# Performance work log

Hardware: AMD Instinct MI355X
Metric: run time of the kernel (lower is better)

## Reference

```python
import jax, jax.numpy as jnp
import numpy as np

B, S, D, H = 2, 2048, 1024, 16
DK = D // H


def setup_inputs() -> dict:
    key = jax.random.key(0)
    ks = jax.random.split(key, 12)
    s = 1.0 / np.sqrt(D)
    return {
        "query": jax.random.normal(ks[0], (B, S, D), dtype=jnp.float32),
        "key": jax.random.normal(ks[1], (B, S, D), dtype=jnp.float32),
        "value": jax.random.normal(ks[2], (B, S, D), dtype=jnp.float32),
        "mask": jax.random.randint(ks[3], (B, 1, 1, S), 0, 2, dtype=jnp.int32),
        "wq": jax.random.normal(ks[4], (D, D), dtype=jnp.float32) * s,
        "bq": jnp.zeros((D,), dtype=jnp.float32),
        "wk": jax.random.normal(ks[5], (D, D), dtype=jnp.float32) * s,
        "bk": jnp.zeros((D,), dtype=jnp.float32),
        "wv": jax.random.normal(ks[6], (D, D), dtype=jnp.float32) * s,
        "bv": jnp.zeros((D,), dtype=jnp.float32),
        "wo": jax.random.normal(ks[7], (D, D), dtype=jnp.float32) * s,
        "bo": jnp.zeros((D,), dtype=jnp.float32),
    }


def reference(query, key, value, mask, wq, bq, wk, bk, wv, bv, wo, bo):
    b, s, d = query.shape
    # torch Linear: y = x @ W^T + b, then split heads -> [B, H, S, dk]
    def proj(x, w, bias):
        return (x @ w.T + bias).reshape(b, -1, H, DK).transpose(0, 2, 1, 3)

    q = proj(query, wq, bq)
    k = proj(key, wk, bk)
    v = proj(value, wv, bv)

    scores = jnp.einsum("bhqd,bhkd->bhqk", q, k) / jnp.sqrt(jnp.float32(DK))
    scores = jnp.where(mask == 0, jnp.float32(-1e9), scores)
    attn = jax.nn.softmax(scores, axis=-1)  # [B,H,S,S]
    x = jnp.einsum("bhqk,bhkd->bhqd", attn, v)
    x = x.transpose(0, 2, 1, 3).reshape(b, s, d)
    return x @ wo.T + bo
```

## Files before the change

### kernel.cpp

```cpp
#include <hip/hip_runtime.h>
#include <math.h>

#define B_  2
#define S_  2048
#define D_  1024
#define H_  16
#define DK_ 64
#define NT_ (S_ / 64)

typedef unsigned short u16;
typedef unsigned int u32;
typedef __bf16 bf16x8 __attribute__((ext_vector_type(8)));
typedef float f32x4 __attribute__((ext_vector_type(4)));

typedef const __attribute__((address_space(1))) void* gas1_t;
typedef __attribute__((address_space(3))) void* las3_t;

__device__ __forceinline__ void gload_lds16(const void* g, void* l) {
    __builtin_amdgcn_global_load_lds((gas1_t)g, (las3_t)l, 16, 0, 0);
}

__device__ __forceinline__ u16 f2bf(float f) {
    union { float f; unsigned u; } v; v.f = f;
    return (u16)((v.u + 0x7fffu + ((v.u >> 16) & 1u)) >> 16);
}

__device__ __forceinline__ u32 pack_bf16_2(float lo, float hi) {
    union { float f; u32 u; } a, b;
    a.f = lo; b.f = hi;
    return __builtin_amdgcn_perm(b.u + 0x8000u, a.u + 0x8000u, 0x07060302u);
}

__global__ __launch_bounds__(256)
void cast_all(const float* __restrict__ q, const float* __restrict__ k,
              const float* __restrict__ v, const float* __restrict__ wq,
              const float* __restrict__ wk, const float* __restrict__ wv,
              const float* __restrict__ wo,
              u16* __restrict__ qb, u16* __restrict__ kb, u16* __restrict__ vb,
              u16* __restrict__ wqb, u16* __restrict__ wkb, u16* __restrict__ wvb,
              u16* __restrict__ wob)
{
    const int i = blockIdx.x * 256 + threadIdx.x;
    const float* src; u16* dst; int off;
    if (i < 3 * 1048576) {
        const int seg = i >> 20; off = i & 1048575;
        src = (seg == 0) ? q : (seg == 1) ? k : v;
        dst = (seg == 0) ? qb : (seg == 1) ? kb : vb;
    } else {
        const int j = i - 3 * 1048576;
        const int seg = j >> 18; off = j & 262143;
        src = (seg == 0) ? wq : (seg == 1) ? wk : (seg == 2) ? wv : wo;
        dst = (seg == 0) ? wqb : (seg == 1) ? wkb : (seg == 2) ? wvb : wob;
    }
    const float4 val = ((const float4*)src)[off];
    uint2 o;
    o.x = pack_bf16_2(val.x, val.y);
    o.y = pack_bf16_2(val.z, val.w);
    ((uint2*)dst)[off] = o;
}

template<int BN>
__device__ __forceinline__ void gemm_body(
    const u16* __restrict__ A, const u16* __restrict__ W,
    const float* __restrict__ bias, void* __restrict__ outp,
    float scale, int mode)
{
    constexpr int NJ = BN / 32;
    __shared__ u16 sA[128 * 32];
    __shared__ u16 sW[BN * 32];

    const int tid  = threadIdx.x;
    const int wave = tid >> 6, lane = tid & 63;
    const int quad = lane >> 4, l16 = lane & 15;
    const int m0 = blockIdx.y * 128;
    const int n0 = blockIdx.x * BN;
    const int wm = (wave >> 1) * 64;
    const int wn = (wave & 1) * (BN / 2);
    const int lrow = lane >> 2;
    const int lcol = (lane & 3) * 8;

    f32x4 acc[4][NJ];
    const f32x4 zero = {0.f, 0.f, 0.f, 0.f};
#pragma unroll
    for (int i = 0; i < 4; ++i)
#pragma unroll
        for (int j = 0; j < NJ; ++j) acc[i][j] = zero;

    for (int k0 = 0; k0 < D_; k0 += 32) {
        const int t0 = wave, t1 = wave + 4;
        gload_lds16(A + (size_t)(m0 + t0 * 16 + lrow) * D_ + k0 + lcol, sA + t0 * 512);
        gload_lds16(A + (size_t)(m0 + t1 * 16 + lrow) * D_ + k0 + lcol, sA + t1 * 512);
        if (BN == 128) {
            gload_lds16(W + (size_t)(n0 + t0 * 16 + lrow) * D_ + k0 + lcol, sW + t0 * 512);
            gload_lds16(W + (size_t)(n0 + t1 * 16 + lrow) * D_ + k0 + lcol, sW + t1 * 512);
        } else {
            gload_lds16(W + (size_t)(n0 + wave * 16 + lrow) * D_ + k0 + lcol, sW + wave * 512);
        }
        __syncthreads();

        bf16x8 af[4], bfr[NJ];
#pragma unroll
        for (int i = 0; i < 4; ++i)
            af[i] = *(const bf16x8*)(sA + (wm + i * 16 + l16) * 32 + quad * 8);
#pragma unroll
        for (int j = 0; j < NJ; ++j)
            bfr[j] = *(const bf16x8*)(sW + (wn + j * 16 + l16) * 32 + quad * 8);
#pragma unroll
        for (int i = 0; i < 4; ++i)
#pragma unroll
            for (int j = 0; j < NJ; ++j)
                acc[i][j] = __builtin_amdgcn_mfma_f32_16x16x32_bf16(af[i], bfr[j], acc[i][j], 0, 0, 0);
        __syncthreads();
    }

#pragma unroll
    for (int i = 0; i < 4; ++i) {
#pragma unroll
        for (int j = 0; j < NJ; ++j) {
            const int n = n0 + wn + j * 16 + l16;
            const float bn = bias[n];
            if (mode == 2) {
                const int mbase = m0 + wm + i * 16 + quad * 4;
                const int b = mbase >> 11, s = mbase & (S_ - 1);
                const int h = n >> 6, dk = n & 63;
                uint2 o;
                o.x = pack_bf16_2(acc[i][j][0] + bn, acc[i][j][1] + bn);
                o.y = pack_bf16_2(acc[i][j][2] + bn, acc[i][j][3] + bn);
                *(uint2*)((u16*)outp + (((size_t)(b * H_ + h)) * DK_ + dk) * S_ + s) = o;
            } else {
#pragma unroll
                for (int r = 0; r < 4; ++r) {
                    const int m = m0 + wm + i * 16 + quad * 4 + r;
                    const float v = acc[i][j][r] + bn;
                    if (mode == 0) {
                        ((float*)outp)[(size_t)m * D_ + n] = v;
                    } else {
                        const u16 hv = f2bf(v * scale);
                        const int b = m >> 11, s = m & (S_ - 1);
                        const int h = n >> 6, dk = n & 63;
                        ((u16*)outp)[(((size_t)(b * H_ + h)) * S_ + s) * DK_ + dk] = hv;
                    }
                }
            }
        }
    }
}

__global__ __launch_bounds__(256)
void qkv_gemm(const u16* __restrict__ qin, const u16* __restrict__ kin, const u16* __restrict__ vin,
              const u16* __restrict__ wqb, const u16* __restrict__ wkb, const u16* __restrict__ wvb,
              const float* __restrict__ bq, const float* __restrict__ bk, const float* __restrict__ bv,
              u16* __restrict__ Qp, u16* __restrict__ Kp, u16* __restrict__ Vp)
{
    const int z = blockIdx.z;
    const u16* A = (z == 0) ? qin : (z == 1) ? kin : vin;
    const u16* W = (z == 0) ? wqb : (z == 1) ? wkb : wvb;
    const float* bias = (z == 0) ? bq : (z == 1) ? bk : bv;
    u16* outp = (z == 0) ? Qp : (z == 1) ? Kp : Vp;
    const float scale = (z == 0) ? 0.18033688011112042f : 1.0f;
    const int mode = (z == 2) ? 2 : 1;
    gemm_body<128>(A, W, bias, outp, scale, mode);
}

__global__ __launch_bounds__(256)
void out_gemm(const u16* __restrict__ Xc, const u16* __restrict__ wob,
              const float* __restrict__ bo, float* __restrict__ out)
{
    gemm_body<128>(Xc, wob, bo, out, 1.0f, 0);
}

__global__ __launch_bounds__(256)
void attn_mfma(const u16* __restrict__ Qp, const u16* __restrict__ Kp,
               const u16* __restrict__ Vt, const int* __restrict__ mask,
               u16* __restrict__ Xc)
{
    __shared__ u16 sQ[128 * 64];
    __shared__ u16 sP[128 * 64];
    __shared__ u16 sK[2][64 * 64];
    __shared__ u16 sV[2][64 * 64];

    const int tid  = threadIdx.x;
    const int wave = tid >> 6, lane = tid & 63;
    const int quad = lane >> 4, l16 = lane & 15;
    const int qt = blockIdx.x & 15;
    const int bh = blockIdx.x >> 4;
    const int b  = bh >> 4;
    const int h  = bh & 15;
    const int srow = lane >> 3;
    const int scol = ((lane & 7) ^ srow) * 8;
    const int sw7  = l16 & 7;

    const u16* Qb = Qp + ((size_t)bh * S_ + qt * 128) * DK_;
    const u16* Kb = Kp + (size_t)bh * S_ * DK_;
    const u16* Vb = Vt + (size_t)bh * DK_ * S_;
    const int* mb = mask + b * S_;

#pragma unroll
    for (int t = 0; t < 4; ++t) {
        const int tt = wave + t * 4;
        gload_lds16(Qb + (size_t)(tt * 8 + srow) * DK_ + scol, sQ + tt * 512);
    }
#pragma unroll
    for (int t = 0; t < 2; ++t) {
        const int tt = wave + t * 4;
        gload_lds16(Kb + (size_t)(tt * 8 + srow) * DK_ + scol, &sK[0][tt * 512]);
        gload_lds16(Vb + (size_t)(tt * 8 + srow) * S_ + scol, &sV[0][tt * 512]);
    }
    __syncthreads();

    bf16x8 qf[2][2];
#pragma unroll
    for (int iq = 0; iq < 2; ++iq)
#pragma unroll
        for (int ks = 0; ks < 2; ++ks) {
            const int row = wave * 32 + iq * 16 + l16;
            const int phys = (ks * 4 + quad) ^ sw7;
            qf[iq][ks] = *(const bf16x8*)(sQ + row * 64 + phys * 8);
        }

    u16* sPw = sP + wave * 2048;

    f32x4 oacc[2][4];
    const f32x4 zero = {0.f, 0.f, 0.f, 0.f};
#pragma unroll
    for (int im = 0; im < 2; ++im)
#pragma unroll
        for (int nd = 0; nd < 4; ++nd) oacc[im][nd] = zero;
    f32x4 lsum4[2] = {zero, zero};

    int4 mk4[4];
#pragma unroll
    for (int in = 0; in < 4; ++in)
        mk4[in] = *(const int4*)(mb + in * 16 + quad * 4);

    for (int kt = 0; kt < NT_; ++kt) {
        __syncthreads();
        const int cur = kt & 1;

        int4 mkn[4];
        const int ktn = (kt < NT_ - 1) ? kt + 1 : kt;
#pragma unroll
        for (int in = 0; in < 4; ++in)
            mkn[in] = *(const int4*)(mb + ktn * 64 + in * 16 + quad * 4);

        f32x4 binit[4];
#pragma unroll
        for (int in = 0; in < 4; ++in) {
            binit[in][0] = mk4[in].x ? 0.f : -1e9f;
            binit[in][1] = mk4[in].y ? 0.f : -1e9f;
            binit[in][2] = mk4[in].z ? 0.f : -1e9f;
            binit[in][3] = mk4[in].w ? 0.f : -1e9f;
        }
        f32x4 sfr[2][4];
#pragma unroll
        for (int iq = 0; iq < 2; ++iq)
#pragma unroll
            for (int in = 0; in < 4; ++in) sfr[iq][in] = binit[in];

#pragma unroll
        for (int in = 0; in < 4; ++in) {
#pragma unroll
            for (int ks = 0; ks < 2; ++ks) {
                const int phys = (ks * 4 + quad) ^ sw7;
                const bf16x8 kf = *(const bf16x8*)(&sK[cur][(in * 16 + l16) * 64 + phys * 8]);
#pragma unroll
                for (int iq = 0; iq < 2; ++iq)
                    sfr[iq][in] = __builtin_amdgcn_mfma_f32_16x16x32_bf16(kf, qf[iq][ks], sfr[iq][in], 0, 0, 0);
            }
        }

#pragma unroll
        for (int iq = 0; iq < 2; ++iq) {
#pragma unroll
            for (int in = 0; in < 4; ++in) {
                const float p0 = __builtin_amdgcn_exp2f(sfr[iq][in][0]);
                const float p1 = __builtin_amdgcn_exp2f(sfr[iq][in][1]);
                const float p2 = __builtin_amdgcn_exp2f(sfr[iq][in][2]);
                const float p3 = __builtin_amdgcn_exp2f(sfr[iq][in][3]);
                lsum4[iq][in] += (p0 + p1) + (p2 + p3);
                uint2 o;
                o.x = pack_bf16_2(p0, p1);
                o.y = pack_bf16_2(p2, p3);
                const int pchunk = (in * 2 + (quad >> 1)) ^ sw7;
                *(uint2*)(sPw + (iq * 16 + l16) * 64 + pchunk * 8 + (quad & 1) * 4) = o;
            }
        }
#pragma unroll
        for (int in = 0; in < 4; ++in) mk4[in] = mkn[in];

        __syncthreads();

        if (kt < NT_ - 1) {
            const int alt = cur ^ 1;
#pragma unroll
            for (int t = 0; t < 2; ++t) {
                const int tt = wave + t * 4;
                gload_lds16(Kb + (size_t)((kt + 1) * 64 + tt * 8 + srow) * DK_ + scol, &sK[alt][tt * 512]);
                gload_lds16(Vb + (size_t)(tt * 8 + srow) * S_ + (kt + 1) * 64 + scol, &sV[alt][tt * 512]);
            }
        }

#pragma unroll
        for (int ks = 0; ks < 2; ++ks) {
            bf16x8 pf[2];
#pragma unroll
            for (int im = 0; im < 2; ++im) {
                const int phys = (ks * 4 + quad) ^ sw7;
                pf[im] = *(const bf16x8*)(sPw + (im * 16 + l16) * 64 + phys * 8);
            }
#pragma unroll
            for (int nd = 0; nd < 4; ++nd) {
                const int phys = (ks * 4 + quad) ^ sw7;
                const bf16x8 vf = *(const bf16x8*)(&sV[cur][(nd * 16 + l16) * 64 + phys * 8]);
#pragma unroll
                for (int im = 0; im < 2; ++im)
                    oacc[im][nd] = __builtin_amdgcn_mfma_f32_16x16x32_bf16(pf[im], vf, oacc[im][nd], 0, 0, 0);
            }
        }
    }

    float lq[2];
#pragma unroll
    for (int iq = 0; iq < 2; ++iq) {
        float v = (lsum4[iq][0] + lsum4[iq][1]) + (lsum4[iq][2] + lsum4[iq][3]);
        v += __shfl_xor(v, 16);
        v += __shfl_xor(v, 32);
        lq[iq] = v;
    }
    float* sL = (float*)sPw;
    if (quad == 0) {
        sL[l16] = lq[0];
        sL[16 + l16] = lq[1];
    }
    float linv[2][4];
#pragma unroll
    for (int im = 0; im < 2; ++im)
#pragma unroll
        for (int r = 0; r < 4; ++r)
            linv[im][r] = __builtin_amdgcn_rcpf(sL[im * 16 + quad * 4 + r]);

#pragma unroll
    for (int im = 0; im < 2; ++im)
#pragma unroll
        for (int r = 0; r < 4; ++r) {
            const int s = qt * 128 + wave * 32 + im * 16 + quad * 4 + r;
            const float inv = linv[im][r];
#pragma unroll
            for (int nd = 0; nd < 4; ++nd)
                Xc[((size_t)(b * S_ + s)) * D_ + h * 64 + nd * 16 + l16] =
                    f2bf(oacc[im][nd][r] * inv);
        }
}

extern "C" void kernel_launch(void* const* d_in, const int* in_sizes, int n_in,
                              void* d_out, int out_size, void* d_ws, size_t ws_size,
                              hipStream_t stream)
{
    (void)in_sizes; (void)n_in; (void)out_size; (void)ws_size;

    const float* query = (const float*)d_in[0];
    const float* key   = (const float*)d_in[1];
    const float* value = (const float*)d_in[2];
    const int*   mask  = (const int*)d_in[3];
    const float* wq    = (const float*)d_in[4];
    const float* bq    = (const float*)d_in[5];
    const float* wk    = (const float*)d_in[6];
    const float* bk    = (const float*)d_in[7];
    const float* wv    = (const float*)d_in[8];
    const float* bv    = (const float*)d_in[9];
    const float* wo    = (const float*)d_in[10];
    const float* bo    = (const float*)d_in[11];

    const size_t NE = (size_t)B_ * S_ * D_;
    const size_t WE = (size_t)D_ * D_;

    u16* qb  = (u16*)d_ws;
    u16* kb  = qb + NE;
    u16* vb  = kb + NE;
    u16* wqb = vb + NE;
    u16* wkb = wqb + WE;
    u16* wvb = wkb + WE;
    u16* wob = wvb + WE;
    u16* Qp  = wob + WE;
    u16* Kp  = Qp + NE;
    u16* Vp  = Kp + NE;
    u16* Xc  = qb;

    cast_all<<<16384, 256, 0, stream>>>(query, key, value, wq, wk, wv, wo,
                                        qb, kb, vb, wqb, wkb, wvb, wob);

    qkv_gemm<<<dim3(D_ / 128, (B_ * S_) / 128, 3), 256, 0, stream>>>(
        qb, kb, vb, wqb, wkb, wvb, bq, bk, bv, Qp, Kp, Vp);

    attn_mfma<<<dim3(B_ * H_ * (S_ / 128)), 256, 0, stream>>>(Qp, Kp, Vp, mask, Xc);

    out_gemm<<<dim3(D_ / 128, (B_ * S_) / 128), 256, 0, stream>>>(Xc, wob, bo, (float*)d_out);
}
```

Before: 250.3 us.

## Transpose V projection via swapped GEMM, precompute mask bias, restructure attention sync

The V projection is now computed as Wv·Vᵀ, so the GEMM writes V already transposed with contiguous rows instead of strided 4-element scatter stores. The mask is converted once to an additive float bias inside the cast kernel, which removes the per-tile int-to-bias selects in attention. The attention kernel reuses the Q shared buffer for P, issues the next K/V prefetch at the top of the loop, and drops one __syncthreads per tile. The output GEMM switches to 64-wide N tiles for more blocks. Reusing sQ for P and moving the prefetch add hazard risk, and the smaller output tile lowers data reuse.

```diff
diff --git a/kernel.cpp b/kernel.cpp
--- a/kernel.cpp
+++ b/kernel.cpp
@@ -35,12 +35,17 @@
 void cast_all(const float* __restrict__ q, const float* __restrict__ k,
               const float* __restrict__ v, const float* __restrict__ wq,
               const float* __restrict__ wk, const float* __restrict__ wv,
-              const float* __restrict__ wo,
+              const float* __restrict__ wo, const int* __restrict__ mask,
               u16* __restrict__ qb, u16* __restrict__ kb, u16* __restrict__ vb,
               u16* __restrict__ wqb, u16* __restrict__ wkb, u16* __restrict__ wvb,
-              u16* __restrict__ wob)
+              u16* __restrict__ wob, float* __restrict__ mbias)
 {
     const int i = blockIdx.x * 256 + threadIdx.x;
+    if (i >= 4194304) {
+        const int idx = i - 4194304;
+        mbias[idx] = mask[idx] ? 0.0f : -1e9f;
+        return;
+    }
     const float* src; u16* dst; int off;
     if (i < 3 * 1048576) {
         const int seg = i >> 20; off = i & 1048575;
@@ -63,7 +68,7 @@
 __device__ __forceinline__ void gemm_body(
     const u16* __restrict__ A, const u16* __restrict__ W,
     const float* __restrict__ bias, void* __restrict__ outp,
-    float scale, int mode)
+    float scale, int mode, int m0, int n0)
 {
     constexpr int NJ = BN / 32;
     __shared__ u16 sA[128 * 32];
@@ -72,8 +77,6 @@
     const int tid  = threadIdx.x;
     const int wave = tid >> 6, lane = tid & 63;
     const int quad = lane >> 4, l16 = lane & 15;
-    const int m0 = blockIdx.y * 128;
-    const int n0 = blockIdx.x * BN;
     const int wm = (wave >> 1) * 64;
     const int wn = (wave & 1) * (BN / 2);
     const int lrow = lane >> 2;
@@ -118,16 +121,14 @@
 #pragma unroll
         for (int j = 0; j < NJ; ++j) {
             const int n = n0 + wn + j * 16 + l16;
-            const float bn = bias[n];
-            if (mode == 2) {
-                const int mbase = m0 + wm + i * 16 + quad * 4;
-                const int b = mbase >> 11, s = mbase & (S_ - 1);
-                const int h = n >> 6, dk = n & 63;
-                uint2 o;
-                o.x = pack_bf16_2(acc[i][j][0] + bn, acc[i][j][1] + bn);
-                o.y = pack_bf16_2(acc[i][j][2] + bn, acc[i][j][3] + bn);
-                *(uint2*)((u16*)outp + (((size_t)(b * H_ + h)) * DK_ + dk) * S_ + s) = o;
+            if (mode == 3) {
+#pragma unroll
+                for (int r = 0; r < 4; ++r) {
+                    const int mp = m0 + wm + i * 16 + quad * 4 + r;
+                    ((u16*)outp)[(size_t)mp * (B_ * S_) + n] = f2bf(acc[i][j][r] + bias[mp]);
+                }
             } else {
+                const float bn = bias[n];
 #pragma unroll
                 for (int r = 0; r < 4; ++r) {
                     const int m = m0 + wm + i * 16 + quad * 4 + r;
@@ -135,10 +136,9 @@
                     if (mode == 0) {
                         ((float*)outp)[(size_t)m * D_ + n] = v;
                     } else {
-                        const u16 hv = f2bf(v * scale);
                         const int b = m >> 11, s = m & (S_ - 1);
                         const int h = n >> 6, dk = n & 63;
-                        ((u16*)outp)[(((size_t)(b * H_ + h)) * S_ + s) * DK_ + dk] = hv;
+                        ((u16*)outp)[(((size_t)(b * H_ + h)) * S_ + s) * DK_ + dk] = f2bf(v * scale);
                     }
                 }
             }
@@ -150,32 +150,34 @@
 void qkv_gemm(const u16* __restrict__ qin, const u16* __restrict__ kin, const u16* __restrict__ vin,
               const u16* __restrict__ wqb, const u16* __restrict__ wkb, const u16* __restrict__ wvb,
               const float* __restrict__ bq, const float* __restrict__ bk, const float* __restrict__ bv,
-              u16* __restrict__ Qp, u16* __restrict__ Kp, u16* __restrict__ Vp)
+              u16* __restrict__ Qp, u16* __restrict__ Kp, u16* __restrict__ Vt)
 {
     const int z = blockIdx.z;
-    const u16* A = (z == 0) ? qin : (z == 1) ? kin : vin;
-    const u16* W = (z == 0) ? wqb : (z == 1) ? wkb : wvb;
-    const float* bias = (z == 0) ? bq : (z == 1) ? bk : bv;
-    u16* outp = (z == 0) ? Qp : (z == 1) ? Kp : Vp;
-    const float scale = (z == 0) ? 0.18033688011112042f : 1.0f;
-    const int mode = (z == 2) ? 2 : 1;
-    gemm_body<128>(A, W, bias, outp, scale, mode);
+    if (z == 2) {
+        gemm_body<128>(wvb, vin, bv, Vt, 1.0f, 3, blockIdx.x * 128, blockIdx.y * 128);
+    } else {
+        const u16* A = (z == 0) ? qin : kin;
+        const u16* W = (z == 0) ? wqb : wkb;
+        const float* bias = (z == 0) ? bq : bk;
+        u16* outp = (z == 0) ? Qp : Kp;
+        const float scale = (z == 0) ? 0.18033688011112042f : 1.0f;
+        gemm_body<128>(A, W, bias, outp, scale, 1, blockIdx.y * 128, blockIdx.x * 128);
+    }
 }
 
 __global__ __launch_bounds__(256)
 void out_gemm(const u16* __restrict__ Xc, const u16* __restrict__ wob,
               const float* __restrict__ bo, float* __restrict__ out)
 {
-    gemm_body<128>(Xc, wob, bo, out, 1.0f, 0);
+    gemm_body<64>(Xc, wob, bo, out, 1.0f, 0, blockIdx.y * 128, blockIdx.x * 64);
 }
 
 __global__ __launch_bounds__(256)
 void attn_mfma(const u16* __restrict__ Qp, const u16* __restrict__ Kp,
-               const u16* __restrict__ Vt, const int* __restrict__ mask,
+               const u16* __restrict__ Vt, const float* __restrict__ mbias,
                u16* __restrict__ Xc)
 {
     __shared__ u16 sQ[128 * 64];
-    __shared__ u16 sP[128 * 64];
     __shared__ u16 sK[2][64 * 64];
     __shared__ u16 sV[2][64 * 64];
 
@@ -192,8 +194,8 @@
 
     const u16* Qb = Qp + ((size_t)bh * S_ + qt * 128) * DK_;
     const u16* Kb = Kp + (size_t)bh * S_ * DK_;
-    const u16* Vb = Vt + (size_t)bh * DK_ * S_;
-    const int* mb = mask + b * S_;
+    const u16* Vb = Vt + ((size_t)h * 64) * (B_ * S_) + b * S_;
+    const float* mbf = mbias + b * S_;
 
 #pragma unroll
     for (int t = 0; t < 4; ++t) {
@@ -204,7 +206,7 @@
     for (int t = 0; t < 2; ++t) {
         const int tt = wave + t * 4;
         gload_lds16(Kb + (size_t)(tt * 8 + srow) * DK_ + scol, &sK[0][tt * 512]);
-        gload_lds16(Vb + (size_t)(tt * 8 + srow) * S_ + scol, &sV[0][tt * 512]);
+        gload_lds16(Vb + (size_t)(tt * 8 + srow) * (B_ * S_) + scol, &sV[0][tt * 512]);
     }
     __syncthreads();
 
@@ -217,8 +219,7 @@
             const int phys = (ks * 4 + quad) ^ sw7;
             qf[iq][ks] = *(const bf16x8*)(sQ + row * 64 + phys * 8);
         }
-
-    u16* sPw = sP + wave * 2048;
+    u16* sPw = sQ + wave * 2048;
 
     f32x4 oacc[2][4];
     const f32x4 zero = {0.f, 0.f, 0.f, 0.f};
@@ -228,34 +229,40 @@
         for (int nd = 0; nd < 4; ++nd) oacc[im][nd] = zero;
     f32x4 lsum4[2] = {zero, zero};
 
-    int4 mk4[4];
+    float4 mk4[4];
 #pragma unroll
     for (int in = 0; in < 4; ++in)
-        mk4[in] = *(const int4*)(mb + in * 16 + quad * 4);
+        mk4[in] = *(const float4*)(mbf + in * 16 + quad * 4);
 
     for (int kt = 0; kt < NT_; ++kt) {
         __syncthreads();
         const int cur = kt & 1;
 
-        int4 mkn[4];
+        if (kt < NT_ - 1) {
+            const int alt = cur ^ 1;
+#pragma unroll
+            for (int t = 0; t < 2; ++t) {
+                const int tt = wave + t * 4;
+                gload_lds16(Kb + (size_t)((kt + 1) * 64 + tt * 8 + srow) * DK_ + scol, &sK[alt][tt * 512]);
+                gload_lds16(Vb + (size_t)(tt * 8 + srow) * (B_ * S_) + (kt + 1) * 64 + scol, &sV[alt][tt * 512]);
+            }
+        }
+        float4 mkn[4];
         const int ktn = (kt < NT_ - 1) ? kt + 1 : kt;
 #pragma unroll
         for (int in = 0; in < 4; ++in)
-            mkn[in] = *(const int4*)(mb + ktn * 64 + in * 16 + quad * 4);
-
-        f32x4 binit[4];
-#pragma unroll
-        for (int in = 0; in < 4; ++in) {
-            binit[in][0] = mk4[in].x ? 0.f : -1e9f;
-            binit[in][1] = mk4[in].y ? 0.f : -1e9f;
-            binit[in][2] = mk4[in].z ? 0.f : -1e9f;
-            binit[in][3] = mk4[in].w ? 0.f : -1e9f;
-        }
+            mkn[in] = *(const float4*)(mbf + ktn * 64 + in * 16 + quad * 4);
+
         f32x4 sfr[2][4];
 #pragma unroll
         for (int iq = 0; iq < 2; ++iq)
 #pragma unroll
-            for (int in = 0; in < 4; ++in) sfr[iq][in] = binit[in];
+            for (int in = 0; in < 4; ++in) {
+                sfr[iq][in][0] = mk4[in].x;
+                sfr[iq][in][1] = mk4[in].y;
+                sfr[iq][in][2] = mk4[in].z;
+                sfr[iq][in][3] = mk4[in].w;
+            }
 
 #pragma unroll
         for (int in = 0; in < 4; ++in) {
@@ -287,18 +294,6 @@
         }
 #pragma unroll
         for (int in = 0; in < 4; ++in) mk4[in] = mkn[in];
-
-        __syncthreads();
-
-        if (kt < NT_ - 1) {
-            const int alt = cur ^ 1;
-#pragma unroll
-            for (int t = 0; t < 2; ++t) {
-                const int tt = wave + t * 4;
-                gload_lds16(Kb + (size_t)((kt + 1) * 64 + tt * 8 + srow) * DK_ + scol, &sK[alt][tt * 512]);
-                gload_lds16(Vb + (size_t)(tt * 8 + srow) * S_ + (kt + 1) * 64 + scol, &sV[alt][tt * 512]);
-            }
-        }
 
 #pragma unroll
         for (int ks = 0; ks < 2; ++ks) {
@@ -383,16 +378,17 @@
     u16* wob = wvb + WE;
     u16* Qp  = wob + WE;
     u16* Kp  = Qp + NE;
-    u16* Vp  = Kp + NE;
+    u16* Vt  = Kp + NE;
+    float* mbias = (float*)(Vt + NE);
     u16* Xc  = qb;
 
-    cast_all<<<16384, 256, 0, stream>>>(query, key, value, wq, wk, wv, wo,
-                                        qb, kb, vb, wqb, wkb, wvb, wob);
+    cast_all<<<16400, 256, 0, stream>>>(query, key, value, wq, wk, wv, wo, mask,
+                                        qb, kb, vb, wqb, wkb, wvb, wob, mbias);
 
     qkv_gemm<<<dim3(D_ / 128, (B_ * S_) / 128, 3), 256, 0, stream>>>(
-        qb, kb, vb, wqb, wkb, wvb, bq, bk, bv, Qp, Kp, Vp);
-
-    attn_mfma<<<dim3(B_ * H_ * (S_ / 128)), 256, 0, stream>>>(Qp, Kp, Vp, mask, Xc);
-
-    out_gemm<<<dim3(D_ / 128, (B_ * S_) / 128), 256, 0, stream>>>(Xc, wob, bo, (float*)d_out);
-}
+        qb, kb, vb, wqb, wkb, wvb, bq, bk, bv, Qp, Kp, Vt);
+
+    attn_mfma<<<dim3(B_ * H_ * (S_ / 128)), 256, 0, stream>>>(Qp, Kp, Vt, mbias, Xc);
+
+    out_gemm<<<dim3(D_ / 64, (B_ * S_) / 128), 256, 0, stream>>>(Xc, wob, bo, (float*)d_out);
+}
```

After: 242.2 us. 3.2% less time.
